# Performance work log

Measured on AMD Instinct MI355X. Metric: run time of the kernel, lower is better.

The kernel has to match this reference:

```python
import jax, jax.numpy as jnp
import numpy as np
from functools import partial

EPS = 1e-5
TOP_K = 1
NUM_EXPERTS = 3
LOSS_COEF = 0.01


def conv2d(x, w, stride, pad):
    return jax.lax.conv_general_dilated(
        x, w, (stride, stride), [(pad, pad), (pad, pad)],
        dimension_numbers=("NCHW", "OIHW", "NCHW"))


def setup_inputs() -> dict:
    key = jax.random.key(0)
    ks = jax.random.split(key, 8)
    b, c, t, h, w = 8, 3, 5, 512, 512
    E = NUM_EXPERTS
    s = 0.05  # small init scale
    return {
        "x": jax.random.normal(ks[0], (b, c, t, h, w), jnp.float32),
        "g_conv_w": jax.random.normal(ks[1], (64, 15, 7, 7), jnp.float32) * s,
        "g_bn_gamma": jnp.ones((64,), jnp.float32),
        "g_bn_beta": jnp.zeros((64,), jnp.float32),
        "g_bn_mean": jnp.zeros((64,), jnp.float32),
        "g_bn_var": jnp.ones((64,), jnp.float32),
        "g_fc_w": jax.random.normal(ks[2], (E, 64), jnp.float32) * s,
        "g_fc_b": jnp.zeros((E,), jnp.float32),
        "e_conv1_w": jax.random.normal(ks[3], (E, 64, 15, 7, 7), jnp.float32) * s,
        "e_conv2_w": jax.random.normal(ks[4], (E, 128, 64, 3, 3), jnp.float32) * s,
        "e_head_w1": jax.random.normal(ks[5], (E, 128, 128, 3, 3), jnp.float32) * s,
        "e_head_b1": jnp.zeros((E, 128), jnp.float32),
        "e_head_w2": jax.random.normal(ks[6], (E, 5, 128, 1, 1), jnp.float32) * s,
        "e_head_b2": jnp.zeros((E, 5), jnp.float32),
    }


def gating(xr, g_conv_w, g_bn_gamma, g_bn_beta, g_bn_mean, g_bn_var, g_fc_w, g_fc_b):
    # backbone: conv 7x7 s2 -> BN (eval) -> ReLU -> maxpool 3x3 s2 -> GAP -> fc
    f = conv2d(xr, g_conv_w, 2, 3)
    scale = g_bn_gamma / jnp.sqrt(g_bn_var + EPS)
    f = f * scale[None, :, None, None] + (g_bn_beta - g_bn_mean * scale)[None, :, None, None]
    f = jax.nn.relu(f)
    f = jax.lax.reduce_window(f, -jnp.inf, jax.lax.max, (1, 1, 3, 3), (1, 1, 2, 2),
                              [(0, 0), (0, 0), (1, 1), (1, 1)])
    pooled = f.mean(axis=(2, 3))                       # (b, 64)
    logits = pooled @ g_fc_w.T + g_fc_b                # (b, E)
    b = logits.shape[0]
    _, top_idx = jax.lax.top_k(logits, TOP_K)          # (b, k)
    rows = jnp.arange(b)[:, None]
    # eval-mode gating: uniform 1/k over selected experts
    sparse_gates = jnp.zeros_like(logits).at[rows, top_idx].set(1.0 / TOP_K)
    expert_mask = jnp.zeros_like(logits).at[rows, top_idx].set(1.0)
    density = expert_mask.mean(axis=0)
    density_proxy = jax.nn.softmax(logits, axis=1).mean(axis=0)
    aux_loss = (density * density_proxy).sum() * NUM_EXPERTS
    return sparse_gates, aux_loss


def expert_forward(xr, w1, w2, hw1, hb1, hw2, hb2):
    y = jax.nn.relu(conv2d(xr, w1, 2, 3))              # (b, 64, H/2, W/2)
    y = jax.nn.relu(conv2d(y, w2, 2, 1))               # (b, 128, H/4, W/4)
    y = jax.nn.relu(conv2d(y, hw1, 1, 1) + hb1[None, :, None, None])
    y = conv2d(y, hw2, 1, 0) + hb2[None, :, None, None]  # (b, 5, H/4, W/4)
    return y


def reference(x, g_conv_w, g_bn_gamma, g_bn_beta, g_bn_mean, g_bn_var, g_fc_w, g_fc_b,
              e_conv1_w, e_conv2_w, e_head_w1, e_head_b1, e_head_w2, e_head_b2):
    b, c, t, h, w = x.shape
    xr = x.reshape(b, c * t, h, w)
    sparse_gates, aux_loss = gating(xr, g_conv_w, g_bn_gamma, g_bn_beta,
                                    g_bn_mean, g_bn_var, g_fc_w, g_fc_b)
    # run all experts (gates are 0 for unselected -> identical math to sparse dispatch)
    outs = jax.vmap(lambda w1, w2, hw1, hb1, hw2, hb2:
                    expert_forward(xr, w1, w2, hw1, hb1, hw2, hb2))(
        e_conv1_w, e_conv2_w, e_head_w1, e_head_b1, e_head_w2, e_head_b2)  # (E,b,5,h4,w4)
    combined = jnp.einsum("ebchw,be->bchw", outs, sparse_gates)
    hm, wh, reg = combined[:, 0:1], combined[:, 1:3], combined[:, 3:5]
    return hm, wh, reg, LOSS_COEF * aux_loss
```

## Files before the change

kernel.cpp:

```cpp
#include <hip/hip_runtime.h>
#include <cstdint>
#include <cmath>


typedef _Float16 f16x8 __attribute__((ext_vector_type(8)));
typedef _Float16 f16x4 __attribute__((ext_vector_type(4)));
typedef float f32x4 __attribute__((ext_vector_type(4)));

__device__ __forceinline__ void g2l16(const void* g, void* l) {
  __builtin_amdgcn_global_load_lds((__attribute__((address_space(1))) void*)g,
                                   (__attribute__((address_space(3))) void*)l,
                                   16, 0, 0);
}

__global__ __launch_bounds__(256) void prep_x_k(
    const float* __restrict__ x, _Float16* __restrict__ xp)
{
  const int t = blockIdx.x * 256 + threadIdx.x;
  const int pix = t & 262143;
  const int b   = t >> 18;
  const float* src = x + (size_t)b * 15 * 262144 + pix;
  f16x8 lo, hi;
#pragma unroll
  for (int c = 0; c < 8; ++c)  lo[c] = (_Float16)src[(size_t)c * 262144];
#pragma unroll
  for (int c = 8; c < 15; ++c) hi[c - 8] = (_Float16)src[(size_t)c * 262144];
  hi[7] = (_Float16)0.f;
  *(f16x8*)&xp[(size_t)t * 16]     = lo;
  *(f16x8*)&xp[(size_t)t * 16 + 8] = hi;
}

__global__ __launch_bounds__(256) void prep_w7_k(
    const float* __restrict__ gw, const float* __restrict__ ew,
    _Float16* __restrict__ wp)
{
  const int i = blockIdx.x * 256 + threadIdx.x;
  const int kk   = i & 31;
  const int cout = (i >> 5) & 63;
  const int pair = (i >> 11) & 3;
  const int v    = i >> 13;
  const int ky = v % 7, set = v / 7;
  const int t = kk >> 4, cin = kk & 15;
  const int kx = 2 * pair + t;
  float val = 0.f;
  if (cin < 15 && kx < 7) {
    if (set == 0) val = gw[((cout * 15 + cin) * 7 + ky) * 7 + kx];
    else          val = ew[((((set - 1) * 64 + cout) * 15 + cin) * 7 + ky) * 7 + kx];
  }
  wp[i] = (_Float16)val;
}

template<int CINC>
__global__ __launch_bounds__(256) void prep_w3_k(
    const float* __restrict__ w, _Float16* __restrict__ wp)
{
  constexpr int CH = CINC / 32;
  const int i = blockIdx.x * 256 + threadIdx.x;
  const int kk   = i & 31;
  const int cout = (i >> 5) & 127;
  int rest = i >> 12;
  const int ch  = rest % CH;  rest /= CH;
  const int tap = rest % 9;
  const int e   = rest / 9;
  const int cin = ch * 32 + kk;
  wp[i] = (_Float16)w[((size_t)(e * 128 + cout) * CINC + cin) * 9 + tap];
}

template<int MODE>
__global__ __launch_bounds__(256, 3) void conv7m_k(
    const _Float16* __restrict__ xp, const _Float16* __restrict__ wp,
    const float* __restrict__ bn_g, const float* __restrict__ bn_b,
    const float* __restrict__ bn_m, const float* __restrict__ bn_v,
    const int* __restrict__ sel, _Float16* __restrict__ out)
{
  constexpr int ROWF = 518 * 16;
  __shared__ __align__(16) _Float16 smem[18432];
  const int oy = blockIdx.x & 255, b = blockIdx.x >> 8;
  const int wv = threadIdx.x >> 6, lane = threadIdx.x & 63;
  const int ln15 = lane & 15, quad = lane >> 4;
  const int npx0 = wv * 64;

  int set = 0;
  if constexpr (MODE == 1) set = 1 + sel[b];
  const _Float16* wset = wp + (size_t)set * (7 * 4 * 64 * 32);
  const _Float16* xb   = xp + (size_t)b * (512 * 512 * 16);

  const _Float16* xrow[7];
  bool rowok[7];
#pragma unroll
  for (int ky = 0; ky < 7; ++ky) {
    const int iy = 2 * oy - 3 + ky;
    rowok[ky] = (unsigned)iy < 512u;
    const int iyc = iy < 0 ? 0 : (iy > 511 ? 511 : iy);
    xrow[ky] = xb + (size_t)iyc * (512 * 16);
  }

  if (threadIdx.x < 32) {
    const int bi = threadIdx.x >> 4, k = threadIdx.x & 15;
    if (k < 12) {
      const int g = (k < 6) ? k : (1030 + k - 6);
      f16x8 z = {};
      *(f16x8*)&smem[bi * ROWF + g * 8] = z;
    }
  }

  f32x4 acc[4][4];
#pragma unroll
  for (int f = 0; f < 4; ++f)
#pragma unroll
    for (int g = 0; g < 4; ++g) acc[f][g] = (f32x4){0.f, 0.f, 0.f, 0.f};

  auto load_af = [&](int t, f16x8* af) {
    const int ky = t >> 2, pair = t & 3;
    const _Float16* wt = wset + (size_t)((ky * 4 + pair) * 64) * 32;
#pragma unroll
    for (int f = 0; f < 4; ++f)
      af[f] = *(const f16x8*)&wt[(f * 16 + ln15) * 32 + quad * 8];
  };
  auto stage = [&](int ky, int bi) {
    _Float16* bufb = &smem[bi * ROWF];
    const _Float16* xr = xrow[ky];
#pragma unroll
    for (int s = 0; s < 4; ++s) {
      const int seg = wv * 4 + s;
      const int gl = 6 + seg * 64 + lane;
      const int gs = gl ^ ((gl >> 3) & 7);
      g2l16(xr + (size_t)((gs >> 1) - 3) * 16 + (gs & 1) * 8,
            bufb + (6 + seg * 64) * 8);
    }
  };

  int gb[4];
#pragma unroll
  for (int g = 0; g < 4; ++g)
    gb[g] = 4 * (npx0 + g * 16 + ln15) + quad;

  f16x8 afA[4], afB[4];
  load_af(0, afA);
  stage(0, 0);
  __syncthreads();

#pragma unroll
  for (int t = 0; t < 28; ++t) {
    const int ky = t >> 2, pair = t & 3;
    const int cur = ky & 1;
    f16x8* afc = (t & 1) ? afB : afA;
    f16x8* afn = (t & 1) ? afA : afB;
    if (t + 1 < 28) load_af(t + 1, afn);
    if (pair == 0 && ky + 1 < 7) stage(ky + 1, cur ^ 1);
    if (rowok[ky]) {
      const _Float16* bufb = &smem[cur * ROWF];
#pragma unroll
      for (int g = 0; g < 4; ++g) {
        const int gq = gb[g] + 4 * pair;
        const int gs = gq ^ ((gq >> 3) & 7);
        const f16x8 bf = *(const f16x8*)&bufb[gs * 8];
#pragma unroll
        for (int f = 0; f < 4; ++f)
          acc[f][g] = __builtin_amdgcn_mfma_f32_16x16x32_f16(afc[f], bf, acc[f][g], 0, 0, 0);
      }
    }
    if (pair == 3) __syncthreads();
  }

  _Float16* sw = &smem[wv * 4608];
#pragma unroll
  for (int f = 0; f < 4; ++f) {
    float scl[4], add[4];
#pragma unroll
    for (int r = 0; r < 4; ++r) {
      const int cout = f * 16 + quad * 4 + r;
      if constexpr (MODE == 0) {
        const float sc = bn_g[cout] * rsqrtf(bn_v[cout] + 1e-5f);
        scl[r] = sc; add[r] = bn_b[cout] - bn_m[cout] * sc;
      } else { scl[r] = 1.f; add[r] = 0.f; }
    }
#pragma unroll
    for (int g = 0; g < 4; ++g) {
      f16x4 h;
#pragma unroll
      for (int r = 0; r < 4; ++r)
        h[r] = (_Float16)fmaxf(acc[f][g][r] * scl[r] + add[r], 0.f);
      *(f16x4*)&sw[(g * 16 + ln15) * 72 + f * 16 + quad * 4] = h;
    }
  }
  __syncthreads();
  const size_t rowbase = ((size_t)(b * 256 + oy) * 256 + npx0) * 64;
#pragma unroll
  for (int i = 0; i < 8; ++i) {
    const int pxl = (lane >> 3) + i * 8;
    const int c8  = (lane & 7) * 8;
    const f16x8 v = *(const f16x8*)&sw[pxl * 72 + c8];
    *(f16x8*)&out[rowbase + (size_t)pxl * 64 + c8] = v;
  }
}

template<int CINC, int S, int INSZ, int OUTSZ, int MODE>
__global__ __launch_bounds__(256, 3) void conv3m_k(
    const _Float16* __restrict__ xp, const _Float16* __restrict__ wp,
    const float* __restrict__ p_bias, const int* __restrict__ sel,
    _Float16* __restrict__ out)
{
  constexpr int CH  = CINC / 32;
  constexpr int NCH = 3 * CH;
  constexpr int NT  = NCH * 3;
  constexpr int NPX = (S == 1) ? (OUTSZ + 2) : (2 * OUTSZ + 1);
  constexpr int ROWF = NPX * 32;
  constexpr int NGR  = NPX * 4;
  constexpr int SPW  = INSZ / 64;
  __shared__ __align__(16) _Float16 smem[18432];
  const int oy = blockIdx.x % OUTSZ, b = blockIdx.x / OUTSZ;
  const int wv = threadIdx.x >> 6, lane = threadIdx.x & 63;
  const int ln15 = lane & 15, quad = lane >> 4;
  const int mwb = (wv >> 1) * 64, nwb = (wv & 1) * 64;

  const int e = sel[b];
  const _Float16* we = wp + (size_t)e * (9 * CH * 128 * 32);
  const _Float16* xb = xp + (size_t)b * ((size_t)INSZ * INSZ * CINC);

  const _Float16* xrow[3];
  bool rowok[3];
#pragma unroll
  for (int ky = 0; ky < 3; ++ky) {
    const int iy = S * oy + ky - 1;
    rowok[ky] = (unsigned)iy < (unsigned)INSZ;
    const int iyc = iy < 0 ? 0 : (iy >= INSZ ? INSZ - 1 : iy);
    xrow[ky] = xb + (size_t)iyc * INSZ * CINC;
  }

  {
    constexpr int HGPB = (S == 1) ? 8 : 4;
    if (threadIdx.x < 2 * HGPB) {
      const int bi = threadIdx.x / HGPB, k = threadIdx.x % HGPB;
      const int g = (k < 4) ? k : (NGR - 8 + k);
      f16x8 z = {};
      *(f16x8*)&smem[bi * ROWF + g * 8] = z;
    }
  }

  f32x4 acc[4][4];
#pragma unroll
  for (int f = 0; f < 4; ++f)
#pragma unroll
    for (int g = 0; g < 4; ++g) acc[f][g] = (f32x4){0.f, 0.f, 0.f, 0.f};

  auto load_af = [&](int t, f16x8* af) {
    const int c = t / 3, kx = t % 3;
    const int ky = c / CH, ch = c % CH;
    const _Float16* wt = we + (size_t)(((ky * 3 + kx) * CH + ch) * 128) * 32;
#pragma unroll
    for (int f = 0; f < 4; ++f)
      af[f] = *(const f16x8*)&wt[(mwb + f * 16 + ln15) * 32 + quad * 8];
  };
  auto stage = [&](int c, int bi) {
    const int ky = c / CH, ch = c % CH;
    _Float16* bufb = &smem[bi * ROWF];
    const _Float16* xr = xrow[ky];
#pragma unroll
    for (int s = 0; s < SPW; ++s) {
      const int seg = wv * SPW + s;
      const int gl = 4 + seg * 64 + lane;
      const int gs = gl ^ ((gl >> 3) & 7);
      g2l16(xr + (size_t)((gs >> 2) - 1) * CINC + ch * 32 + (gs & 3) * 8,
            bufb + (4 + seg * 64) * 8);
    }
  };

  int gb[4];
#pragma unroll
  for (int g = 0; g < 4; ++g) {
    const int ox = nwb + g * 16 + ln15;
    gb[g] = 4 * S * ox + quad;
  }

  f16x8 afA[4], afB[4];
  load_af(0, afA);
  stage(0, 0);
  __syncthreads();

#pragma unroll
  for (int t = 0; t < NT; ++t) {
    const int c = t / 3, kx = t % 3;
    const int ky = c / CH;
    const int cur = c & 1;
    f16x8* afc = (t & 1) ? afB : afA;
    f16x8* afn = (t & 1) ? afA : afB;
    if (t + 1 < NT) load_af(t + 1, afn);
    if (kx == 0 && c + 1 < NCH) stage(c + 1, cur ^ 1);
    if (rowok[ky]) {
      const _Float16* bufb = &smem[cur * ROWF];
#pragma unroll
      for (int g = 0; g < 4; ++g) {
        const int gq = gb[g] + 4 * kx;
        const int gs = gq ^ ((gq >> 3) & 7);
        const f16x8 bf = *(const f16x8*)&bufb[gs * 8];
#pragma unroll
        for (int f = 0; f < 4; ++f)
          acc[f][g] = __builtin_amdgcn_mfma_f32_16x16x32_f16(afc[f], bf, acc[f][g], 0, 0, 0);
      }
    }
    if (kx == 2) __syncthreads();
  }

  _Float16* sw = &smem[wv * 4608];
#pragma unroll
  for (int f = 0; f < 4; ++f) {
#pragma unroll
    for (int g = 0; g < 4; ++g) {
      f16x4 h;
#pragma unroll
      for (int r = 0; r < 4; ++r) {
        const int cout = mwb + f * 16 + quad * 4 + r;
        float v = acc[f][g][r];
        if constexpr (MODE == 2) v += p_bias[e * 128 + cout];
        h[r] = (_Float16)fmaxf(v, 0.f);
      }
      *(f16x4*)&sw[(g * 16 + ln15) * 72 + f * 16 + quad * 4] = h;
    }
  }
  __syncthreads();
  const size_t rowbase = ((size_t)(b * OUTSZ + oy) * OUTSZ + nwb) * 128 + mwb;
#pragma unroll
  for (int i = 0; i < 8; ++i) {
    const int pxl = (lane >> 3) + i * 8;
    const int c8  = (lane & 7) * 8;
    const f16x8 v = *(const f16x8*)&sw[pxl * 72 + c8];
    *(f16x8*)&out[rowbase + (size_t)pxl * 128 + c8] = v;
  }
}

__global__ void zero_k(float* __restrict__ pooled) {
  if (threadIdx.x < 512) pooled[threadIdx.x] = 0.f;
}

__global__ __launch_bounds__(256) void pool_k(
    const _Float16* __restrict__ f, float* __restrict__ pooled)
{
  const int b  = blockIdx.x >> 7;
  const int py = blockIdx.x & 127;
  const int wv = threadIdx.x >> 6, lane = threadIdx.x & 63;
  const int c8  = (lane & 7) * 8;
  const int pxq = lane >> 3;
  const _Float16* fb = f + (size_t)b * 256 * 256 * 64;

  const int y0 = 2 * py - 1;
  float s[8];
#pragma unroll
  for (int j = 0; j < 8; ++j) s[j] = 0.f;

#pragma unroll
  for (int step = 0; step < 4; ++step) {
    const int px = wv * 32 + step * 8 + pxq;
    const int x0 = 2 * px - 1;
    f16x8 m;
#pragma unroll
    for (int j = 0; j < 8; ++j) m[j] = (_Float16)(-60000.f);
#pragma unroll
    for (int dy = 0; dy < 3; ++dy) {
      const int y = y0 + dy;
      if ((unsigned)y < 256u) {
        const _Float16* row = fb + (size_t)y * 256 * 64 + c8;
        if (x0 >= 0)
          m = __builtin_elementwise_max(m, *(const f16x8*)&row[(size_t)x0 * 64]);
        m = __builtin_elementwise_max(m, *(const f16x8*)&row[(size_t)(x0 + 1) * 64]);
        m = __builtin_elementwise_max(m, *(const f16x8*)&row[(size_t)(x0 + 2) * 64]);
      }
    }
#pragma unroll
    for (int j = 0; j < 8; ++j) s[j] += (float)m[j];
  }

  __shared__ float red[256][8];
#pragma unroll
  for (int j = 0; j < 8; ++j) red[threadIdx.x][j] = s[j];
  __syncthreads();
  if (threadIdx.x < 64) {
    const int c = threadIdx.x, cg = c >> 3, cj = c & 7;
    float t = 0.f;
#pragma unroll
    for (int k = 0; k < 32; ++k)
      t += red[(k >> 3) * 64 + (k & 7) * 8 + cg][cj];
    atomicAdd(&pooled[b * 64 + c], t);
  }
}

__global__ __launch_bounds__(64) void gate_k(
    const float* __restrict__ pooled, const float* __restrict__ fcw,
    const float* __restrict__ fcb, int* __restrict__ sel, float* __restrict__ out_aux)
{
  __shared__ float probs[8][3];
  __shared__ int sidx[8];
  const int b = threadIdx.x;
  if (b < 8) {
    float l[3];
#pragma unroll
    for (int e = 0; e < 3; ++e) {
      float s = fcb[e];
      for (int c = 0; c < 64; ++c)
        s = fmaf(pooled[b * 64 + c] * (1.f / 16384.f), fcw[e * 64 + c], s);
      l[e] = s;
    }
    int best = 0;
    if (l[1] > l[best]) best = 1;
    if (l[2] > l[best]) best = 2;
    sel[b] = best;
    sidx[b] = best;
    const float m = fmaxf(l[0], fmaxf(l[1], l[2]));
    const float e0 = expf(l[0] - m), e1 = expf(l[1] - m), e2 = expf(l[2] - m);
    const float inv = 1.f / (e0 + e1 + e2);
    probs[b][0] = e0 * inv; probs[b][1] = e1 * inv; probs[b][2] = e2 * inv;
  }
  __syncthreads();
  if (threadIdx.x == 0) {
    float cnt[3] = {0.f, 0.f, 0.f}, pr[3] = {0.f, 0.f, 0.f};
    for (int bb = 0; bb < 8; ++bb) {
      cnt[sidx[bb]] += 1.f;
#pragma unroll
      for (int e = 0; e < 3; ++e) pr[e] += probs[bb][e];
    }
    float aux = 0.f;
#pragma unroll
    for (int e = 0; e < 3; ++e) aux += (cnt[e] * 0.125f) * (pr[e] * 0.125f);
    *out_aux = 0.01f * (3.f * aux);
  }
}

__global__ __launch_bounds__(256) void head2m_k(
    const _Float16* __restrict__ in, const float* __restrict__ w,
    const float* __restrict__ b2, const int* __restrict__ sel,
    float* __restrict__ out)
{
  const int b = blockIdx.x >> 6;
  const int p = ((blockIdx.x & 63) << 8) + threadIdx.x;
  const int e = sel[b];
  const float* wp = w + (size_t)e * 5 * 128;
  const _Float16* ip = in + ((size_t)(b << 14) + p) * 128;
  float a0 = 0.f, a1 = 0.f, a2 = 0.f, a3 = 0.f, a4 = 0.f;
#pragma unroll
  for (int cc = 0; cc < 16; ++cc) {
    const f16x8 v8 = *(const f16x8*)&ip[cc * 8];
#pragma unroll
    for (int j = 0; j < 8; ++j) {
      const float v = (float)v8[j];
      const int c = cc * 8 + j;
      a0 = fmaf(v, wp[c], a0);
      a1 = fmaf(v, wp[128 + c], a1);
      a2 = fmaf(v, wp[256 + c], a2);
      a3 = fmaf(v, wp[384 + c], a3);
      a4 = fmaf(v, wp[512 + c], a4);
    }
  }
  a0 += b2[e * 5 + 0]; a1 += b2[e * 5 + 1]; a2 += b2[e * 5 + 2];
  a3 += b2[e * 5 + 3]; a4 += b2[e * 5 + 4];
  out[(b << 14) + p] = a0;
  out[131072 + ((b * 2 + 0) << 14) + p] = a1;
  out[131072 + ((b * 2 + 1) << 14) + p] = a2;
  out[393216 + ((b * 2 + 0) << 14) + p] = a3;
  out[393216 + ((b * 2 + 1) << 14) + p] = a4;
}

extern "C" void kernel_launch(void* const* d_in, const int* in_sizes, int n_in,
                              void* d_out, int out_size, void* d_ws, size_t ws_size,
                              hipStream_t stream) {
  const float* x          = (const float*)d_in[0];
  const float* g_conv_w   = (const float*)d_in[1];
  const float* g_bn_gamma = (const float*)d_in[2];
  const float* g_bn_beta  = (const float*)d_in[3];
  const float* g_bn_mean  = (const float*)d_in[4];
  const float* g_bn_var   = (const float*)d_in[5];
  const float* g_fc_w     = (const float*)d_in[6];
  const float* g_fc_b     = (const float*)d_in[7];
  const float* e_conv1_w  = (const float*)d_in[8];
  const float* e_conv2_w  = (const float*)d_in[9];
  const float* e_head_w1  = (const float*)d_in[10];
  const float* e_head_b1  = (const float*)d_in[11];
  const float* e_head_w2  = (const float*)d_in[12];
  const float* e_head_b2  = (const float*)d_in[13];
  float* out = (float*)d_out;

  _Float16* xp      = (_Float16*)d_ws;
  _Float16* featbuf = xp + 33554432;
  _Float16* y2      = featbuf + 33554432;
  _Float16* w7p     = y2 + 16777216;
  _Float16* w2p     = w7p + 229376;
  _Float16* w3p     = w2p + 221184;
  _Float16* y3      = xp;
  float*    pooled  = (float*)(w3p + 442368);
  int*      sel     = (int*)(pooled + 512);

  prep_x_k<<<8192, 256, 0, stream>>>(x, xp);
  prep_w7_k<<<896, 256, 0, stream>>>(g_conv_w, e_conv1_w, w7p);
  prep_w3_k<64><<<864, 256, 0, stream>>>(e_conv2_w, w2p);
  prep_w3_k<128><<<1728, 256, 0, stream>>>(e_head_w1, w3p);
  zero_k<<<1, 512, 0, stream>>>(pooled);

  conv7m_k<0><<<2048, 256, 0, stream>>>(xp, w7p, g_bn_gamma, g_bn_beta,
                                        g_bn_mean, g_bn_var, nullptr, featbuf);
  pool_k<<<1024, 256, 0, stream>>>(featbuf, pooled);
  gate_k<<<1, 64, 0, stream>>>(pooled, g_fc_w, g_fc_b, sel, out + 655360);

  conv7m_k<1><<<2048, 256, 0, stream>>>(xp, w7p, nullptr, nullptr, nullptr, nullptr,
                                        sel, featbuf);
  conv3m_k<64, 2, 256, 128, 1><<<1024, 256, 0, stream>>>(featbuf, w2p, nullptr, sel, y2);
  conv3m_k<128, 1, 128, 128, 2><<<1024, 256, 0, stream>>>(y2, w3p, e_head_b1, sel, y3);
  head2m_k<<<512, 256, 0, stream>>>(y3, e_head_w2, e_head_b2, sel, out);
}
```

Measured before the change: 503.4 us.

## Compute two output rows per block to share staged input rows

```diff
diff --git a/kernel.cpp b/kernel.cpp
--- a/kernel.cpp
+++ b/kernel.cpp
@@ -67,7 +67,7 @@
 }
 
 template<int MODE>
-__global__ __launch_bounds__(256, 3) void conv7m_k(
+__global__ __launch_bounds__(512, 4) void conv7m_k(
     const _Float16* __restrict__ xp, const _Float16* __restrict__ wp,
     const float* __restrict__ bn_g, const float* __restrict__ bn_b,
     const float* __restrict__ bn_m, const float* __restrict__ bn_v,
@@ -75,24 +75,26 @@
 {
   constexpr int ROWF = 518 * 16;
   __shared__ __align__(16) _Float16 smem[18432];
-  const int oy = blockIdx.x & 255, b = blockIdx.x >> 8;
+  const int oy0 = (blockIdx.x & 127) * 2, b = blockIdx.x >> 7;
   const int wv = threadIdx.x >> 6, lane = threadIdx.x & 63;
   const int ln15 = lane & 15, quad = lane >> 4;
-  const int npx0 = wv * 64;
+  const int rw   = wv >> 2;
+  const int npx0 = (wv & 3) * 64;
 
   int set = 0;
   if constexpr (MODE == 1) set = 1 + sel[b];
   const _Float16* wset = wp + (size_t)set * (7 * 4 * 64 * 32);
   const _Float16* xb   = xp + (size_t)b * (512 * 512 * 16);
 
-  const _Float16* xrow[7];
-  bool rowok[7];
-#pragma unroll
-  for (int ky = 0; ky < 7; ++ky) {
-    const int iy = 2 * oy - 3 + ky;
-    rowok[ky] = (unsigned)iy < 512u;
+  const _Float16* xrow[9];
+  bool rowok[9];
+  const int iyb = 2 * oy0 - 3;
+#pragma unroll
+  for (int d = 0; d < 9; ++d) {
+    const int iy = iyb + d;
+    rowok[d] = (unsigned)iy < 512u;
     const int iyc = iy < 0 ? 0 : (iy > 511 ? 511 : iy);
-    xrow[ky] = xb + (size_t)iyc * (512 * 16);
+    xrow[d] = xb + (size_t)iyc * (512 * 16);
   }
 
   if (threadIdx.x < 32) {
@@ -110,19 +112,24 @@
 #pragma unroll
     for (int g = 0; g < 4; ++g) acc[f][g] = (f32x4){0.f, 0.f, 0.f, 0.f};
 
+  auto activ = [&](int t) {
+    const int ky = (t >> 2) - 2 * rw;
+    return ky >= 0 && ky <= 6;
+  };
   auto load_af = [&](int t, f16x8* af) {
-    const int ky = t >> 2, pair = t & 3;
+    const int d = t >> 2, pair = t & 3;
+    const int ky = d - 2 * rw;
     const _Float16* wt = wset + (size_t)((ky * 4 + pair) * 64) * 32;
 #pragma unroll
     for (int f = 0; f < 4; ++f)
       af[f] = *(const f16x8*)&wt[(f * 16 + ln15) * 32 + quad * 8];
   };
-  auto stage = [&](int ky, int bi) {
+  auto stage = [&](int d, int bi) {
     _Float16* bufb = &smem[bi * ROWF];
-    const _Float16* xr = xrow[ky];
-#pragma unroll
-    for (int s = 0; s < 4; ++s) {
-      const int seg = wv * 4 + s;
+    const _Float16* xr = xrow[d];
+#pragma unroll
+    for (int s = 0; s < 2; ++s) {
+      const int seg = wv * 2 + s;
       const int gl = 6 + seg * 64 + lane;
       const int gs = gl ^ ((gl >> 3) & 7);
       g2l16(xr + (size_t)((gs >> 1) - 3) * 16 + (gs & 1) * 8,
@@ -136,19 +143,19 @@
     gb[g] = 4 * (npx0 + g * 16 + ln15) + quad;
 
   f16x8 afA[4], afB[4];
-  load_af(0, afA);
+  if (activ(0)) load_af(0, afA);
   stage(0, 0);
   __syncthreads();
 
 #pragma unroll
-  for (int t = 0; t < 28; ++t) {
-    const int ky = t >> 2, pair = t & 3;
-    const int cur = ky & 1;
+  for (int t = 0; t < 36; ++t) {
+    const int d = t >> 2, pair = t & 3;
+    const int cur = d & 1;
     f16x8* afc = (t & 1) ? afB : afA;
     f16x8* afn = (t & 1) ? afA : afB;
-    if (t + 1 < 28) load_af(t + 1, afn);
-    if (pair == 0 && ky + 1 < 7) stage(ky + 1, cur ^ 1);
-    if (rowok[ky]) {
+    if (t + 1 < 36 && activ(t + 1)) load_af(t + 1, afn);
+    if (pair == 0 && d + 1 < 9) stage(d + 1, cur ^ 1);
+    if (rowok[d] && activ(t)) {
       const _Float16* bufb = &smem[cur * ROWF];
 #pragma unroll
       for (int g = 0; g < 4; ++g) {
@@ -163,69 +170,79 @@
     if (pair == 3) __syncthreads();
   }
 
-  _Float16* sw = &smem[wv * 4608];
-#pragma unroll
-  for (int f = 0; f < 4; ++f) {
-    float scl[4], add[4];
-#pragma unroll
-    for (int r = 0; r < 4; ++r) {
-      const int cout = f * 16 + quad * 4 + r;
-      if constexpr (MODE == 0) {
-        const float sc = bn_g[cout] * rsqrtf(bn_v[cout] + 1e-5f);
-        scl[r] = sc; add[r] = bn_b[cout] - bn_m[cout] * sc;
-      } else { scl[r] = 1.f; add[r] = 0.f; }
-    }
-#pragma unroll
-    for (int g = 0; g < 4; ++g) {
-      f16x4 h;
-#pragma unroll
-      for (int r = 0; r < 4; ++r)
-        h[r] = (_Float16)fmaxf(acc[f][g][r] * scl[r] + add[r], 0.f);
-      *(f16x4*)&sw[(g * 16 + ln15) * 72 + f * 16 + quad * 4] = h;
-    }
-  }
-  __syncthreads();
-  const size_t rowbase = ((size_t)(b * 256 + oy) * 256 + npx0) * 64;
-#pragma unroll
-  for (int i = 0; i < 8; ++i) {
-    const int pxl = (lane >> 3) + i * 8;
-    const int c8  = (lane & 7) * 8;
-    const f16x8 v = *(const f16x8*)&sw[pxl * 72 + c8];
-    *(f16x8*)&out[rowbase + (size_t)pxl * 64 + c8] = v;
+  _Float16* sw = &smem[(wv & 3) * 4608];
+#pragma unroll
+  for (int p = 0; p < 2; ++p) {
+    if (rw == p) {
+#pragma unroll
+      for (int f = 0; f < 4; ++f) {
+        float scl[4], add[4];
+#pragma unroll
+        for (int r = 0; r < 4; ++r) {
+          const int cout = f * 16 + quad * 4 + r;
+          if constexpr (MODE == 0) {
+            const float sc = bn_g[cout] * rsqrtf(bn_v[cout] + 1e-5f);
+            scl[r] = sc; add[r] = bn_b[cout] - bn_m[cout] * sc;
+          } else { scl[r] = 1.f; add[r] = 0.f; }
+        }
+#pragma unroll
+        for (int g = 0; g < 4; ++g) {
+          f16x4 h;
+#pragma unroll
+          for (int r = 0; r < 4; ++r)
+            h[r] = (_Float16)fmaxf(acc[f][g][r] * scl[r] + add[r], 0.f);
+          *(f16x4*)&sw[(g * 16 + ln15) * 72 + f * 16 + quad * 4] = h;
+        }
+      }
+    }
+    __syncthreads();
+    if (rw == p) {
+      const size_t rowbase = ((size_t)(b * 256 + oy0 + p) * 256 + npx0) * 64;
+#pragma unroll
+      for (int i = 0; i < 8; ++i) {
+        const int pxl = (lane >> 3) + i * 8;
+        const int c8  = (lane & 7) * 8;
+        const f16x8 v = *(const f16x8*)&sw[pxl * 72 + c8];
+        *(f16x8*)&out[rowbase + (size_t)pxl * 64 + c8] = v;
+      }
+    }
+    if (p == 0) __syncthreads();
   }
 }
 
 template<int CINC, int S, int INSZ, int OUTSZ, int MODE>
-__global__ __launch_bounds__(256, 3) void conv3m_k(
+__global__ __launch_bounds__(512, 4) void conv3m_k(
     const _Float16* __restrict__ xp, const _Float16* __restrict__ wp,
     const float* __restrict__ p_bias, const int* __restrict__ sel,
     _Float16* __restrict__ out)
 {
-  constexpr int CH  = CINC / 32;
-  constexpr int NCH = 3 * CH;
-  constexpr int NT  = NCH * 3;
-  constexpr int NPX = (S == 1) ? (OUTSZ + 2) : (2 * OUTSZ + 1);
+  constexpr int CH   = CINC / 32;
+  constexpr int R    = (S == 1) ? 4 : 5;
+  constexpr int NCH2 = R * CH;
+  constexpr int NT   = NCH2 * 3;
+  constexpr int NPX  = (S == 1) ? (OUTSZ + 2) : (2 * OUTSZ + 1);
   constexpr int ROWF = NPX * 32;
   constexpr int NGR  = NPX * 4;
-  constexpr int SPW  = INSZ / 64;
+  constexpr int SPW  = (INSZ * 4) / 512;
   __shared__ __align__(16) _Float16 smem[18432];
-  const int oy = blockIdx.x % OUTSZ, b = blockIdx.x / OUTSZ;
+  const int oy0 = (blockIdx.x % (OUTSZ / 2)) * 2, b = blockIdx.x / (OUTSZ / 2);
   const int wv = threadIdx.x >> 6, lane = threadIdx.x & 63;
   const int ln15 = lane & 15, quad = lane >> 4;
-  const int mwb = (wv >> 1) * 64, nwb = (wv & 1) * 64;
+  const int rw  = wv >> 2;
+  const int mwb = ((wv >> 1) & 1) * 64, nwb = (wv & 1) * 64;
 
   const int e = sel[b];
   const _Float16* we = wp + (size_t)e * (9 * CH * 128 * 32);
   const _Float16* xb = xp + (size_t)b * ((size_t)INSZ * INSZ * CINC);
 
-  const _Float16* xrow[3];
-  bool rowok[3];
-#pragma unroll
-  for (int ky = 0; ky < 3; ++ky) {
-    const int iy = S * oy + ky - 1;
-    rowok[ky] = (unsigned)iy < (unsigned)INSZ;
+  const _Float16* xrow[R];
+  bool rowok[R];
+#pragma unroll
+  for (int d = 0; d < R; ++d) {
+    const int iy = S * oy0 + d - 1;
+    rowok[d] = (unsigned)iy < (unsigned)INSZ;
     const int iyc = iy < 0 ? 0 : (iy >= INSZ ? INSZ - 1 : iy);
-    xrow[ky] = xb + (size_t)iyc * INSZ * CINC;
+    xrow[d] = xb + (size_t)iyc * INSZ * CINC;
   }
 
   {
@@ -244,18 +261,23 @@
 #pragma unroll
     for (int g = 0; g < 4; ++g) acc[f][g] = (f32x4){0.f, 0.f, 0.f, 0.f};
 
+  auto activ = [&](int t) {
+    const int ky = (t / 3) / CH - S * rw;
+    return ky >= 0 && ky <= 2;
+  };
   auto load_af = [&](int t, f16x8* af) {
     const int c = t / 3, kx = t % 3;
-    const int ky = c / CH, ch = c % CH;
+    const int d = c / CH, ch = c % CH;
+    const int ky = d - S * rw;
     const _Float16* wt = we + (size_t)(((ky * 3 + kx) * CH + ch) * 128) * 32;
 #pragma unroll
     for (int f = 0; f < 4; ++f)
       af[f] = *(const f16x8*)&wt[(mwb + f * 16 + ln15) * 32 + quad * 8];
   };
   auto stage = [&](int c, int bi) {
-    const int ky = c / CH, ch = c % CH;
+    const int d = c / CH, ch = c % CH;
     _Float16* bufb = &smem[bi * ROWF];
-    const _Float16* xr = xrow[ky];
+    const _Float16* xr = xrow[d];
 #pragma unroll
     for (int s = 0; s < SPW; ++s) {
       const int seg = wv * SPW + s;
@@ -274,20 +296,20 @@
   }
 
   f16x8 afA[4], afB[4];
-  load_af(0, afA);
+  if (activ(0)) load_af(0, afA);
   stage(0, 0);
   __syncthreads();
 
 #pragma unroll
   for (int t = 0; t < NT; ++t) {
     const int c = t / 3, kx = t % 3;
-    const int ky = c / CH;
+    const int d = c / CH;
     const int cur = c & 1;
     f16x8* afc = (t & 1) ? afB : afA;
     f16x8* afn = (t & 1) ? afA : afB;
-    if (t + 1 < NT) load_af(t + 1, afn);
-    if (kx == 0 && c + 1 < NCH) stage(c + 1, cur ^ 1);
-    if (rowok[ky]) {
+    if (t + 1 < NT && activ(t + 1)) load_af(t + 1, afn);
+    if (kx == 0 && c + 1 < NCH2) stage(c + 1, cur ^ 1);
+    if (rowok[d] && activ(t)) {
       const _Float16* bufb = &smem[cur * ROWF];
 #pragma unroll
       for (int g = 0; g < 4; ++g) {
@@ -302,30 +324,38 @@
     if (kx == 2) __syncthreads();
   }
 
-  _Float16* sw = &smem[wv * 4608];
-#pragma unroll
-  for (int f = 0; f < 4; ++f) {
-#pragma unroll
-    for (int g = 0; g < 4; ++g) {
-      f16x4 h;
-#pragma unroll
-      for (int r = 0; r < 4; ++r) {
-        const int cout = mwb + f * 16 + quad * 4 + r;
-        float v = acc[f][g][r];
-        if constexpr (MODE == 2) v += p_bias[e * 128 + cout];
-        h[r] = (_Float16)fmaxf(v, 0.f);
-      }
-      *(f16x4*)&sw[(g * 16 + ln15) * 72 + f * 16 + quad * 4] = h;
-    }
-  }
-  __syncthreads();
-  const size_t rowbase = ((size_t)(b * OUTSZ + oy) * OUTSZ + nwb) * 128 + mwb;
-#pragma unroll
-  for (int i = 0; i < 8; ++i) {
-    const int pxl = (lane >> 3) + i * 8;
-    const int c8  = (lane & 7) * 8;
-    const f16x8 v = *(const f16x8*)&sw[pxl * 72 + c8];
-    *(f16x8*)&out[rowbase + (size_t)pxl * 128 + c8] = v;
+  _Float16* sw = &smem[(wv & 3) * 4608];
+#pragma unroll
+  for (int p = 0; p < 2; ++p) {
+    if (rw == p) {
+#pragma unroll
+      for (int f = 0; f < 4; ++f) {
+#pragma unroll
+        for (int g = 0; g < 4; ++g) {
+          f16x4 h;
+#pragma unroll
+          for (int r = 0; r < 4; ++r) {
+            const int cout = mwb + f * 16 + quad * 4 + r;
+            float v = acc[f][g][r];
+            if constexpr (MODE == 2) v += p_bias[e * 128 + cout];
+            h[r] = (_Float16)fmaxf(v, 0.f);
+          }
+          *(f16x4*)&sw[(g * 16 + ln15) * 72 + f * 16 + quad * 4] = h;
+        }
+      }
+    }
+    __syncthreads();
+    if (rw == p) {
+      const size_t rowbase = ((size_t)(b * OUTSZ + oy0 + p) * OUTSZ + nwb) * 128 + mwb;
+#pragma unroll
+      for (int i = 0; i < 8; ++i) {
+        const int pxl = (lane >> 3) + i * 8;
+        const int c8  = (lane & 7) * 8;
+        const f16x8 v = *(const f16x8*)&sw[pxl * 72 + c8];
+        *(f16x8*)&out[rowbase + (size_t)pxl * 128 + c8] = v;
+      }
+    }
+    if (p == 0) __syncthreads();
   }
 }
 
@@ -494,14 +524,14 @@
   prep_w3_k<128><<<1728, 256, 0, stream>>>(e_head_w1, w3p);
   zero_k<<<1, 512, 0, stream>>>(pooled);
 
-  conv7m_k<0><<<2048, 256, 0, stream>>>(xp, w7p, g_bn_gamma, g_bn_beta,
+  conv7m_k<0><<<1024, 512, 0, stream>>>(xp, w7p, g_bn_gamma, g_bn_beta,
                                         g_bn_mean, g_bn_var, nullptr, featbuf);
   pool_k<<<1024, 256, 0, stream>>>(featbuf, pooled);
   gate_k<<<1, 64, 0, stream>>>(pooled, g_fc_w, g_fc_b, sel, out + 655360);
 
-  conv7m_k<1><<<2048, 256, 0, stream>>>(xp, w7p, nullptr, nullptr, nullptr, nullptr,
+  conv7m_k<1><<<1024, 512, 0, stream>>>(xp, w7p, nullptr, nullptr, nullptr, nullptr,
                                         sel, featbuf);
-  conv3m_k<64, 2, 256, 128, 1><<<1024, 256, 0, stream>>>(featbuf, w2p, nullptr, sel, y2);
-  conv3m_k<128, 1, 128, 128, 2><<<1024, 256, 0, stream>>>(y2, w3p, e_head_b1, sel, y3);
+  conv3m_k<64, 2, 256, 128, 1><<<512, 512, 0, stream>>>(featbuf, w2p, nullptr, sel, y2);
+  conv3m_k<128, 1, 128, 128, 2><<<512, 512, 0, stream>>>(y2, w3p, e_head_b1, sel, y3);
   head2m_k<<<512, 256, 0, stream>>>(y3, e_head_w2, e_head_b2, sel, out);
 }
```

After: 543.2 us. +7.9%, slower.
